# Kernel tuning notes

Measured on AMD Instinct MI355X. Metric: run time of the kernel, lower is better.

Reference implementation:

```python
import math
import jax, jax.numpy as jnp
import numpy as np

IN_DIM = 128
OUT_DIM = 128
D_TIME = 64
N_SRC = 50000
N_DST = 50000
E = 800000
SCALE = math.sqrt(2 * OUT_DIM + D_TIME)  # sqrt(attn_input_dim)


def setup_inputs() -> dict:
    key = jax.random.key(0)
    k1, k2, k3, k4, k5, k6, k7 = jax.random.split(key, 7)
    h_src = jax.random.normal(k1, (N_SRC, IN_DIM), dtype=jnp.float32)
    h_dst = jax.random.normal(k2, (N_DST, IN_DIM), dtype=jnp.float32)
    edge_index = jax.random.randint(k3, (2, E), 0, N_DST, dtype=jnp.int32)
    phi_dt = jax.random.normal(k4, (E, D_TIME), dtype=jnp.float32)
    # parameters (Kaiming-ish scaling like nn.Linear defaults)
    W_src = jax.random.normal(k5, (OUT_DIM, IN_DIM), dtype=jnp.float32) / math.sqrt(IN_DIM)
    W_dst = jax.random.normal(k6, (OUT_DIM, IN_DIM), dtype=jnp.float32) / math.sqrt(IN_DIM)
    attn_w = jax.random.normal(k7, (2 * OUT_DIM + D_TIME,), dtype=jnp.float32) / math.sqrt(2 * OUT_DIM + D_TIME)
    return {"h_src": h_src, "h_dst": h_dst, "edge_index": edge_index,
            "phi_dt": phi_dt, "W_src": W_src, "W_dst": W_dst, "attn_w": attn_w}


def reference(h_src, h_dst, edge_index, phi_dt, W_src, W_dst, attn_w):
    num_dst = h_dst.shape[0]
    src_idx, dst_idx = edge_index[0], edge_index[1]
    # gather + per-edge linear projections: [E, out_dim]
    z_s = h_src[src_idx] @ W_src.T
    z_d = h_dst[dst_idx] @ W_dst.T
    # attn(cat([z_s, z_d, phi])) == z_s@a_s + z_d@a_d + phi@a_t (avoids concat)
    a_s = attn_w[:OUT_DIM]
    a_d = attn_w[OUT_DIM:2 * OUT_DIM]
    a_t = attn_w[2 * OUT_DIM:]
    e = z_s @ a_s + z_d @ a_d + phi_dt @ a_t  # [E]
    e = jax.nn.leaky_relu(e, 0.2) / SCALE
    # numerically stable segment softmax over dst neighbourhoods
    seg_max = jax.ops.segment_max(e, dst_idx, num_segments=num_dst)
    ex = jnp.exp(e - seg_max[dst_idx])
    seg_sum = jax.ops.segment_sum(ex, dst_idx, num_segments=num_dst)
    alpha = ex / (seg_sum[dst_idx] + 1e-12)
    # dropout is identity at inference
    msg = alpha[:, None] * z_s  # [E, out_dim]
    out = jax.ops.segment_sum(msg, dst_idx, num_segments=num_dst)  # [N_dst, out_dim]
    return out
```

## Files before the change

kernel.cpp:

```cpp
#include <hip/hip_runtime.h>
#include <hip/hip_fp16.h>
#include <math.h>

#define IN_DIM   128
#define OUT_DIM  128
#define D_TIME   64
#define NSRC     50000
#define NDST     50000
#define NE       800000
#define NPB      40
#define GR       4
#define NR       (NPB/GR)
#define DPB      16
#define SLOTS    64
#define EPB      256
#define INV_SCALE 0.05590169943749474f

__global__ __launch_bounds__(256) void k_prevec(const float* __restrict__ Wd,
                                                const float* __restrict__ attn,
                                                float* __restrict__ v_d){
    int wv = threadIdx.x >> 6, lane = threadIdx.x & 63;
    int k = blockIdx.x * 4 + wv;
    int j = 2 * lane;
    float acc = Wd[(size_t)j*IN_DIM + k] * attn[OUT_DIM + j]
              + Wd[(size_t)(j+1)*IN_DIM + k] * attn[OUT_DIM + j + 1];
    #pragma unroll
    for (int off = 32; off > 0; off >>= 1) acc += __shfl_down(acc, off, 64);
    if (lane == 0) v_d[k] = acc;
}

__global__ __launch_bounds__(256, 4) void k_front(const float* __restrict__ h_src,
                                                  const float* __restrict__ h_dst,
                                                  const float* __restrict__ W,
                                                  const float* __restrict__ attn,
                                                  const float* __restrict__ v_d,
                                                  __half* __restrict__ Zh,
                                                  float* __restrict__ s_src,
                                                  float* __restrict__ s_dst,
                                                  int* __restrict__ counts){
    int t = threadIdx.x;
    if (blockIdx.x < NSRC/NPB){
        __shared__ float hbuf[2][GR][IN_DIM];
        __shared__ float sred[2][4][GR];
        int r  = t >> 1;
        int kh = t & 1;
        int wv = t >> 6, lane = t & 63;
        float a_r = attn[r];
        float4 wreg[16];
        const float4* wvp = (const float4*)(W + (size_t)r * IN_DIM + kh * 64);
        #pragma unroll
        for (int i = 0; i < 16; ++i) wreg[i] = wvp[i];
        int base = blockIdx.x * NPB;
        ((float2*)hbuf[0][wv])[lane] =
            ((const float2*)(h_src + (size_t)(base + wv)*IN_DIM))[lane];
        for (int rnd = 0; rnd < NR; ++rnd){
            __syncthreads();
            if (rnd + 1 < NR)
                ((float2*)hbuf[(rnd+1)&1][wv])[lane] =
                    ((const float2*)(h_src + (size_t)(base + (rnd+1)*GR + wv)*IN_DIM))[lane];
            if (rnd > 0 && t < GR){
                int pb = (rnd-1)&1;
                s_src[base + (rnd-1)*GR + t] =
                    0.5f*(sred[pb][0][t]+sred[pb][1][t]+sred[pb][2][t]+sred[pb][3][t]);
            }
            #pragma unroll
            for (int g = 0; g < GR; ++g){
                const float* hc = hbuf[rnd&1][g] + kh*64;
                float acc = 0.f;
                #pragma unroll
                for (int i = 0; i < 16; ++i){
                    float4 w = wreg[i]; int k = i*4;
                    acc += hc[k+0]*w.x + hc[k+1]*w.y + hc[k+2]*w.z + hc[k+3]*w.w;
                }
                acc += __shfl_xor(acc, 1, 64);
                if (!kh) Zh[(size_t)(base+rnd*GR+g)*OUT_DIM + r] = __float2half_rn(acc);
                float c = acc * a_r;
                #pragma unroll
                for (int off = 32; off > 0; off >>= 1) c += __shfl_xor(c, off, 64);
                if (lane == 0) sred[rnd&1][wv][g] = c;
            }
        }
        __syncthreads();
        if (t < GR){
            int pb = (NR-1)&1;
            s_src[base + (NR-1)*GR + t] =
                0.5f*(sred[pb][0][t]+sred[pb][1][t]+sred[pb][2][t]+sred[pb][3][t]);
        }
    } else {
        __shared__ float vd[IN_DIM];
        int b = blockIdx.x - NSRC/NPB;
        if (t < IN_DIM) vd[t] = v_d[t];
        __syncthreads();
        int wv = t >> 6, lane = t & 63;
        float v0 = vd[2*lane], v1 = vd[2*lane+1];
        int n0 = b * DPB + wv;
        float2 u[4];
        #pragma unroll
        for (int it = 0; it < 4; ++it)
            u[it] = ((const float2*)(h_dst + (size_t)(n0 + it*4)*IN_DIM))[lane];
        #pragma unroll
        for (int it = 0; it < 4; ++it){
            float acc = u[it].x*v0 + u[it].y*v1;
            #pragma unroll
            for (int off = 32; off > 0; off >>= 1) acc += __shfl_down(acc, off, 64);
            if (lane == 0){
                s_dst[n0 + it*4] = acc;
                counts[n0 + it*4] = 0;
            }
        }
    }
}

__global__ __launch_bounds__(256) void k_edge(const float* __restrict__ phi,
                                              const float* __restrict__ attn,
                                              const int* __restrict__ ei,
                                              const float* __restrict__ s_src,
                                              const float* __restrict__ s_dst,
                                              int2* __restrict__ slots,
                                              int* __restrict__ counts){
    __shared__ float at[D_TIME];
    __shared__ float pts[EPB];
    int t = threadIdx.x;
    if (t < D_TIME) at[t] = attn[2*OUT_DIM + t];
    __syncthreads();
    int sub = t & 15, g = t >> 4;
    int e0 = blockIdx.x * EPB + g;
    float a0 = at[sub*4+0], a1 = at[sub*4+1], a2 = at[sub*4+2], a3 = at[sub*4+3];
    #pragma unroll
    for (int pp = 0; pp < 16; pp += 8){
        float4 w[8];
        #pragma unroll
        for (int q = 0; q < 8; ++q)
            w[q] = ((const float4*)(phi + (size_t)(e0 + (pp+q)*16) * D_TIME))[sub];
        #pragma unroll
        for (int q = 0; q < 8; ++q){
            float acc = w[q].x*a0 + w[q].y*a1 + w[q].z*a2 + w[q].w*a3;
            #pragma unroll
            for (int off = 8; off > 0; off >>= 1) acc += __shfl_xor(acc, off, 64);
            if (sub == 0) pts[g + (pp+q)*16] = acc;
        }
    }
    __syncthreads();
    int e = blockIdx.x * EPB + t;
    int src = ei[e], dst = ei[NE + e];
    float v = s_src[src] + s_dst[dst] + pts[t];
    v = (v > 0.f) ? v : 0.2f * v;
    v *= INV_SCALE;
    int k = atomicAdd(&counts[dst], 1);
    if (k < SLOTS) slots[(dst << 6) + k] = make_int2(src, __float_as_int(v));
}

__global__ __launch_bounds__(256) void k_agg(const int* __restrict__ counts,
                                             const int2* __restrict__ slots,
                                             const __half* __restrict__ Zh,
                                             float* __restrict__ out){
    int wv = threadIdx.x >> 6, lane = threadIdx.x & 63;
    int half = lane >> 5, sl = lane & 31;
    int d = blockIdx.x * 4 + wv;
    int cnt = counts[d]; cnt = (cnt > SLOTS) ? SLOTS : cnt;
    float e = -1e30f; int src = 0;
    if (lane < cnt){
        int2 s = slots[(d << 6) + lane];
        src = s.x; e = __int_as_float(s.y);
    }
    float m = e;
    #pragma unroll
    for (int off = 32; off > 0; off >>= 1) m = fmaxf(m, __shfl_xor(m, off, 64));
    float ex = (lane < cnt) ? __expf(e - m) : 0.f;
    float sum = ex;
    #pragma unroll
    for (int off = 32; off > 0; off >>= 1) sum += __shfl_xor(sum, off, 64);
    float alpha = ex / (sum + 1e-12f);
    float4 acc4 = make_float4(0.f, 0.f, 0.f, 0.f);
    int jmax = (cnt + 7) & ~7;
    for (int j = 0; j < jmax; j += 8){
        float a[4]; int s[4];
        #pragma unroll
        for (int q = 0; q < 4; ++q){
            int idx = j + 2*q + half;
            a[q] = __shfl(alpha, idx, 64);
            s[q] = __shfl(src,   idx, 64);
        }
        float2 raw[4];
        #pragma unroll
        for (int q = 0; q < 4; ++q)
            raw[q] = ((const float2*)(Zh + (size_t)s[q] * OUT_DIM))[sl];
        #pragma unroll
        for (int q = 0; q < 4; ++q){
            __half2 h0 = *(__half2*)&raw[q].x;
            __half2 h1 = *(__half2*)&raw[q].y;
            float2 f0 = __half22float2(h0);
            float2 f1 = __half22float2(h1);
            acc4.x += a[q]*f0.x; acc4.y += a[q]*f0.y;
            acc4.z += a[q]*f1.x; acc4.w += a[q]*f1.y;
        }
    }
    acc4.x += __shfl_xor(acc4.x, 32, 64);
    acc4.y += __shfl_xor(acc4.y, 32, 64);
    acc4.z += __shfl_xor(acc4.z, 32, 64);
    acc4.w += __shfl_xor(acc4.w, 32, 64);
    if (!half) ((float4*)(out + (size_t)d * OUT_DIM))[sl] = acc4;
}

extern "C" void kernel_launch(void* const* d_in, const int* in_sizes, int n_in,
                              void* d_out, int out_size, void* d_ws, size_t ws_size,
                              hipStream_t stream){
    const float* h_src = (const float*)d_in[0];
    const float* h_dst = (const float*)d_in[1];
    const int*   ei    = (const int*)d_in[2];
    const float* phi   = (const float*)d_in[3];
    const float* Wsrc  = (const float*)d_in[4];
    const float* Wdst  = (const float*)d_in[5];
    const float* attn  = (const float*)d_in[6];
    float* out = (float*)d_out;

    char* p = (char*)d_ws;
    auto alloc = [&](size_t bytes)->char*{
        char* r = p; p += (bytes + 255) / 256 * 256; return r;
    };
    __half* Zh   = (__half*)alloc((size_t)NSRC*OUT_DIM*2);
    float* s_src = (float*)alloc((size_t)NSRC*4);
    float* s_dst = (float*)alloc((size_t)NDST*4);
    float* v_d   = (float*)alloc(128*4);
    int2*  slots = (int2*)alloc((size_t)NDST*SLOTS*8);
    int*   counts= (int*)alloc((size_t)NDST*4);

    k_prevec<<<32, 256, 0, stream>>>(Wdst, attn, v_d);
    k_front<<<NSRC/NPB + NDST/DPB, 256, 0, stream>>>(
        h_src, h_dst, Wsrc, attn, v_d, Zh, s_src, s_dst, counts);
    k_edge<<<NE/EPB, 256, 0, stream>>>(phi, attn, ei, s_src, s_dst, slots, counts);
    k_agg<<<NDST/4, 256, 0, stream>>>(counts, slots, Zh, out);
}
```

Before: 449.7 us.

## Move phi time-projection into front kernel and interleave block roles

The per-edge phi·a_t dot product moves out of the edge kernel into the front kernel. Front blocks are interleaved in stripes of 12 (2 src-projection, 5 phi, 5 dst blocks), so bandwidth-heavy phi reads overlap with the compute-heavy src projection. The edge kernel becomes a slim slot-scatter kernel that handles two edges per thread and reads the precomputed pt from a new 3.2MB workspace buffer. This adds an extra write and read of the per-edge scalar in exchange for better overlap and a lighter scatter pass.

```diff
diff --git a/kernel.cpp b/kernel.cpp
--- a/kernel.cpp
+++ b/kernel.cpp
@@ -12,8 +12,8 @@
 #define GR       4
 #define NR       (NPB/GR)
 #define DPB      16
+#define EPB      256
 #define SLOTS    64
-#define EPB      256
 #define INV_SCALE 0.05590169943749474f
 
 __global__ __launch_bounds__(256) void k_prevec(const float* __restrict__ Wd,
@@ -29,19 +29,23 @@
     if (lane == 0) v_d[k] = acc;
 }
 
-__global__ __launch_bounds__(256, 4) void k_front(const float* __restrict__ h_src,
-                                                  const float* __restrict__ h_dst,
-                                                  const float* __restrict__ W,
-                                                  const float* __restrict__ attn,
-                                                  const float* __restrict__ v_d,
-                                                  __half* __restrict__ Zh,
-                                                  float* __restrict__ s_src,
-                                                  float* __restrict__ s_dst,
-                                                  int* __restrict__ counts){
+__global__ __launch_bounds__(256, 4) void k_mega(const float* __restrict__ h_src,
+                                                 const float* __restrict__ h_dst,
+                                                 const float* __restrict__ W,
+                                                 const float* __restrict__ attn,
+                                                 const float* __restrict__ v_d,
+                                                 const float* __restrict__ phi,
+                                                 __half* __restrict__ Zh,
+                                                 float* __restrict__ s_src,
+                                                 float* __restrict__ s_dst,
+                                                 float* __restrict__ pt,
+                                                 int* __restrict__ counts){
     int t = threadIdx.x;
-    if (blockIdx.x < NSRC/NPB){
+    int stripe = blockIdx.x / 12, rem = blockIdx.x % 12;
+    if (rem < 2){
         __shared__ float hbuf[2][GR][IN_DIM];
         __shared__ float sred[2][4][GR];
+        int tb = stripe * 2 + rem;
         int r  = t >> 1;
         int kh = t & 1;
         int wv = t >> 6, lane = t & 63;
@@ -50,7 +54,7 @@
         const float4* wvp = (const float4*)(W + (size_t)r * IN_DIM + kh * 64);
         #pragma unroll
         for (int i = 0; i < 16; ++i) wreg[i] = wvp[i];
-        int base = blockIdx.x * NPB;
+        int base = tb * NPB;
         ((float2*)hbuf[0][wv])[lane] =
             ((const float2*)(h_src + (size_t)(base + wv)*IN_DIM))[lane];
         for (int rnd = 0; rnd < NR; ++rnd){
@@ -86,14 +90,36 @@
             s_src[base + (NR-1)*GR + t] =
                 0.5f*(sred[pb][0][t]+sred[pb][1][t]+sred[pb][2][t]+sred[pb][3][t]);
         }
+    } else if (rem < 7){
+        __shared__ float at[D_TIME];
+        int sb = stripe * 5 + (rem - 2);
+        if (t < D_TIME) at[t] = attn[2*OUT_DIM + t];
+        __syncthreads();
+        int sub = t & 15, g = t >> 4;
+        int e0 = sb * EPB + g;
+        float a0 = at[sub*4+0], a1 = at[sub*4+1], a2 = at[sub*4+2], a3 = at[sub*4+3];
+        #pragma unroll
+        for (int pp = 0; pp < 16; pp += 8){
+            float4 w[8];
+            #pragma unroll
+            for (int q = 0; q < 8; ++q)
+                w[q] = ((const float4*)(phi + (size_t)(e0 + (pp+q)*16) * D_TIME))[sub];
+            #pragma unroll
+            for (int q = 0; q < 8; ++q){
+                float acc = w[q].x*a0 + w[q].y*a1 + w[q].z*a2 + w[q].w*a3;
+                #pragma unroll
+                for (int off = 8; off > 0; off >>= 1) acc += __shfl_xor(acc, off, 64);
+                if (sub == 0) pt[e0 + (pp+q)*16] = acc;
+            }
+        }
     } else {
         __shared__ float vd[IN_DIM];
-        int b = blockIdx.x - NSRC/NPB;
+        int db = stripe * 5 + (rem - 7);
         if (t < IN_DIM) vd[t] = v_d[t];
         __syncthreads();
         int wv = t >> 6, lane = t & 63;
         float v0 = vd[2*lane], v1 = vd[2*lane+1];
-        int n0 = b * DPB + wv;
+        int n0 = db * DPB + wv;
         float2 u[4];
         #pragma unroll
         for (int it = 0; it < 4; ++it)
@@ -111,43 +137,33 @@
     }
 }
 
-__global__ __launch_bounds__(256) void k_edge(const float* __restrict__ phi,
-                                              const float* __restrict__ attn,
-                                              const int* __restrict__ ei,
+__global__ __launch_bounds__(256) void k_slot(const int* __restrict__ ei,
+                                              const float* __restrict__ pt,
                                               const float* __restrict__ s_src,
                                               const float* __restrict__ s_dst,
                                               int2* __restrict__ slots,
                                               int* __restrict__ counts){
-    __shared__ float at[D_TIME];
-    __shared__ float pts[EPB];
-    int t = threadIdx.x;
-    if (t < D_TIME) at[t] = attn[2*OUT_DIM + t];
-    __syncthreads();
-    int sub = t & 15, g = t >> 4;
-    int e0 = blockIdx.x * EPB + g;
-    float a0 = at[sub*4+0], a1 = at[sub*4+1], a2 = at[sub*4+2], a3 = at[sub*4+3];
-    #pragma unroll
-    for (int pp = 0; pp < 16; pp += 8){
-        float4 w[8];
-        #pragma unroll
-        for (int q = 0; q < 8; ++q)
-            w[q] = ((const float4*)(phi + (size_t)(e0 + (pp+q)*16) * D_TIME))[sub];
-        #pragma unroll
-        for (int q = 0; q < 8; ++q){
-            float acc = w[q].x*a0 + w[q].y*a1 + w[q].z*a2 + w[q].w*a3;
-            #pragma unroll
-            for (int off = 8; off > 0; off >>= 1) acc += __shfl_xor(acc, off, 64);
-            if (sub == 0) pts[g + (pp+q)*16] = acc;
-        }
-    }
-    __syncthreads();
-    int e = blockIdx.x * EPB + t;
-    int src = ei[e], dst = ei[NE + e];
-    float v = s_src[src] + s_dst[dst] + pts[t];
-    v = (v > 0.f) ? v : 0.2f * v;
-    v *= INV_SCALE;
-    int k = atomicAdd(&counts[dst], 1);
-    if (k < SLOTS) slots[(dst << 6) + k] = make_int2(src, __float_as_int(v));
+    int base = blockIdx.x * 512 + threadIdx.x;
+    int srcs[2], dsts[2]; float ptv[2]; bool ok[2];
+    #pragma unroll
+    for (int q = 0; q < 2; ++q){
+        int e = base + q*256;
+        ok[q] = (e < NE);
+        int ec = ok[q] ? e : 0;
+        srcs[q] = ei[ec]; dsts[q] = ei[NE + ec]; ptv[q] = pt[ec];
+    }
+    float ss[2], sd[2];
+    #pragma unroll
+    for (int q = 0; q < 2; ++q){ ss[q] = s_src[srcs[q]]; sd[q] = s_dst[dsts[q]]; }
+    #pragma unroll
+    for (int q = 0; q < 2; ++q){
+        if (!ok[q]) continue;
+        float v = ss[q] + sd[q] + ptv[q];
+        v = (v > 0.f) ? v : 0.2f * v;
+        v *= INV_SCALE;
+        int k = atomicAdd(&counts[dsts[q]], 1);
+        if (k < SLOTS) slots[(dsts[q] << 6) + k] = make_int2(srcs[q], __float_as_int(v));
+    }
 }
 
 __global__ __launch_bounds__(256) void k_agg(const int* __restrict__ counts,
@@ -222,12 +238,13 @@
     float* s_src = (float*)alloc((size_t)NSRC*4);
     float* s_dst = (float*)alloc((size_t)NDST*4);
     float* v_d   = (float*)alloc(128*4);
+    float* pt    = (float*)alloc((size_t)NE*4);
     int2*  slots = (int2*)alloc((size_t)NDST*SLOTS*8);
     int*   counts= (int*)alloc((size_t)NDST*4);
 
     k_prevec<<<32, 256, 0, stream>>>(Wdst, attn, v_d);
-    k_front<<<NSRC/NPB + NDST/DPB, 256, 0, stream>>>(
-        h_src, h_dst, Wsrc, attn, v_d, Zh, s_src, s_dst, counts);
-    k_edge<<<NE/EPB, 256, 0, stream>>>(phi, attn, ei, s_src, s_dst, slots, counts);
+    k_mega<<<7500, 256, 0, stream>>>(h_src, h_dst, Wsrc, attn, v_d, phi,
+                                     Zh, s_src, s_dst, pt, counts);
+    k_slot<<<(NE + 511)/512, 256, 0, stream>>>(ei, pt, s_src, s_dst, slots, counts);
     k_agg<<<NDST/4, 256, 0, stream>>>(counts, slots, Zh, out);
 }
```

Result: slower. 490.0 us (+9.0%).

## Stream h_src from global in front kernel and prefetch Zh rows before softmax

Applied to the files above, without the earlier changes.

The src-projection path stops staging rows through shared memory with per-round barriers. Each thread now streams its half of h_src directly from global with software prefetch into four partial accumulators, and the attention-score reduction is deferred to a single end-of-block pass. In the aggregation kernel, the first 16 Zh rows are gathered before the softmax reductions so their load latency overlaps the shuffles, and the remaining loop moves 16 edges per iteration. The dst path reads v_d directly without shared memory. The extra prefetch registers and the duplicated global reads of h_src (two threads per row half) may raise register pressure and cache traffic.

```diff
diff --git a/kernel.cpp b/kernel.cpp
--- a/kernel.cpp
+++ b/kernel.cpp
@@ -9,11 +9,9 @@
 #define NDST     50000
 #define NE       800000
 #define NPB      40
-#define GR       4
-#define NR       (NPB/GR)
 #define DPB      16
+#define EPB      256
 #define SLOTS    64
-#define EPB      256
 #define INV_SCALE 0.05590169943749474f
 
 __global__ __launch_bounds__(256) void k_prevec(const float* __restrict__ Wd,
@@ -40,8 +38,7 @@
                                                   int* __restrict__ counts){
     int t = threadIdx.x;
     if (blockIdx.x < NSRC/NPB){
-        __shared__ float hbuf[2][GR][IN_DIM];
-        __shared__ float sred[2][4][GR];
+        __shared__ float sred[4][NPB];
         int r  = t >> 1;
         int kh = t & 1;
         int wv = t >> 6, lane = t & 63;
@@ -51,48 +48,42 @@
         #pragma unroll
         for (int i = 0; i < 16; ++i) wreg[i] = wvp[i];
         int base = blockIdx.x * NPB;
-        ((float2*)hbuf[0][wv])[lane] =
-            ((const float2*)(h_src + (size_t)(base + wv)*IN_DIM))[lane];
-        for (int rnd = 0; rnd < NR; ++rnd){
-            __syncthreads();
-            if (rnd + 1 < NR)
-                ((float2*)hbuf[(rnd+1)&1][wv])[lane] =
-                    ((const float2*)(h_src + (size_t)(base + (rnd+1)*GR + wv)*IN_DIM))[lane];
-            if (rnd > 0 && t < GR){
-                int pb = (rnd-1)&1;
-                s_src[base + (rnd-1)*GR + t] =
-                    0.5f*(sred[pb][0][t]+sred[pb][1][t]+sred[pb][2][t]+sred[pb][3][t]);
+        for (int n = 0; n < NPB; ++n){
+            const float4* hp = (const float4*)(h_src + (size_t)(base+n)*IN_DIM + kh*64);
+            float4 x[4], y[4];
+            #pragma unroll
+            for (int i = 0; i < 4; ++i) x[i] = hp[i];
+            float a0 = 0.f, a1 = 0.f, a2 = 0.f, a3 = 0.f;
+            #pragma unroll
+            for (int c = 0; c < 4; ++c){
+                if (c + 1 < 4){
+                    #pragma unroll
+                    for (int i = 0; i < 4; ++i) y[i] = hp[(c+1)*4 + i];
+                }
+                #pragma unroll
+                for (int i = 0; i < 4; ++i){
+                    float4 w = wreg[c*4 + i], xv = x[i];
+                    a0 += xv.x*w.x; a1 += xv.y*w.y;
+                    a2 += xv.z*w.z; a3 += xv.w*w.w;
+                }
+                #pragma unroll
+                for (int i = 0; i < 4; ++i) x[i] = y[i];
             }
-            #pragma unroll
-            for (int g = 0; g < GR; ++g){
-                const float* hc = hbuf[rnd&1][g] + kh*64;
-                float acc = 0.f;
-                #pragma unroll
-                for (int i = 0; i < 16; ++i){
-                    float4 w = wreg[i]; int k = i*4;
-                    acc += hc[k+0]*w.x + hc[k+1]*w.y + hc[k+2]*w.z + hc[k+3]*w.w;
-                }
-                acc += __shfl_xor(acc, 1, 64);
-                if (!kh) Zh[(size_t)(base+rnd*GR+g)*OUT_DIM + r] = __float2half_rn(acc);
-                float c = acc * a_r;
-                #pragma unroll
-                for (int off = 32; off > 0; off >>= 1) c += __shfl_xor(c, off, 64);
-                if (lane == 0) sred[rnd&1][wv][g] = c;
-            }
+            float full = (a0 + a1) + (a2 + a3);
+            full += __shfl_xor(full, 1, 64);
+            if (!kh) Zh[(size_t)(base+n)*OUT_DIM + r] = __float2half_rn(full);
+            float c = full * a_r;
+            #pragma unroll
+            for (int off = 2; off <= 32; off <<= 1) c += __shfl_xor(c, off, 64);
+            if (lane == 0) sred[wv][n] = c;
         }
         __syncthreads();
-        if (t < GR){
-            int pb = (NR-1)&1;
-            s_src[base + (NR-1)*GR + t] =
-                0.5f*(sred[pb][0][t]+sred[pb][1][t]+sred[pb][2][t]+sred[pb][3][t]);
-        }
+        if (t < NPB)
+            s_src[base + t] = sred[0][t] + sred[1][t] + sred[2][t] + sred[3][t];
     } else {
-        __shared__ float vd[IN_DIM];
         int b = blockIdx.x - NSRC/NPB;
-        if (t < IN_DIM) vd[t] = v_d[t];
-        __syncthreads();
         int wv = t >> 6, lane = t & 63;
-        float v0 = vd[2*lane], v1 = vd[2*lane+1];
+        float2 vv = ((const float2*)v_d)[lane];
         int n0 = b * DPB + wv;
         float2 u[4];
         #pragma unroll
@@ -100,7 +91,7 @@
             u[it] = ((const float2*)(h_dst + (size_t)(n0 + it*4)*IN_DIM))[lane];
         #pragma unroll
         for (int it = 0; it < 4; ++it){
-            float acc = u[it].x*v0 + u[it].y*v1;
+            float acc = u[it].x*vv.x + u[it].y*vv.y;
             #pragma unroll
             for (int off = 32; off > 0; off >>= 1) acc += __shfl_down(acc, off, 64);
             if (lane == 0){
@@ -163,6 +154,13 @@
         int2 s = slots[(d << 6) + lane];
         src = s.x; e = __int_as_float(s.y);
     }
+    int sidx[8];
+    #pragma unroll
+    for (int q = 0; q < 8; ++q) sidx[q] = __shfl(src, 2*q + half, 64);
+    float2 raw[8];
+    #pragma unroll
+    for (int q = 0; q < 8; ++q)
+        raw[q] = ((const float2*)(Zh + (size_t)sidx[q] * OUT_DIM))[sl];
     float m = e;
     #pragma unroll
     for (int off = 32; off > 0; off >>= 1) m = fmaxf(m, __shfl_xor(m, off, 64));
@@ -172,23 +170,33 @@
     for (int off = 32; off > 0; off >>= 1) sum += __shfl_xor(sum, off, 64);
     float alpha = ex / (sum + 1e-12f);
     float4 acc4 = make_float4(0.f, 0.f, 0.f, 0.f);
-    int jmax = (cnt + 7) & ~7;
-    for (int j = 0; j < jmax; j += 8){
-        float a[4]; int s[4];
-        #pragma unroll
-        for (int q = 0; q < 4; ++q){
+    #pragma unroll
+    for (int q = 0; q < 8; ++q){
+        float a = __shfl(alpha, 2*q + half, 64);
+        __half2 h0 = *(__half2*)&raw[q].x;
+        __half2 h1 = *(__half2*)&raw[q].y;
+        float2 f0 = __half22float2(h0);
+        float2 f1 = __half22float2(h1);
+        acc4.x += a*f0.x; acc4.y += a*f0.y;
+        acc4.z += a*f1.x; acc4.w += a*f1.y;
+    }
+    int jmax = (cnt + 15) & ~15;
+    for (int j = 16; j < jmax; j += 16){
+        float a[8]; int s[8];
+        #pragma unroll
+        for (int q = 0; q < 8; ++q){
             int idx = j + 2*q + half;
             a[q] = __shfl(alpha, idx, 64);
             s[q] = __shfl(src,   idx, 64);
         }
-        float2 raw[4];
-        #pragma unroll
-        for (int q = 0; q < 4; ++q)
-            raw[q] = ((const float2*)(Zh + (size_t)s[q] * OUT_DIM))[sl];
-        #pragma unroll
-        for (int q = 0; q < 4; ++q){
-            __half2 h0 = *(__half2*)&raw[q].x;
-            __half2 h1 = *(__half2*)&raw[q].y;
+        float2 r2[8];
+        #pragma unroll
+        for (int q = 0; q < 8; ++q)
+            r2[q] = ((const float2*)(Zh + (size_t)s[q] * OUT_DIM))[sl];
+        #pragma unroll
+        for (int q = 0; q < 8; ++q){
+            __half2 h0 = *(__half2*)&r2[q].x;
+            __half2 h1 = *(__half2*)&r2[q].y;
             float2 f0 = __half22float2(h0);
             float2 f1 = __half22float2(h1);
             acc4.x += a[q]*f0.x; acc4.y += a[q]*f0.y;
```

New measurement: 588.4 us. 30.8% more time.
